# Optimization experiments

Measured on AMD Instinct MI355X. Metric: run time of the kernel, lower is better.

The kernel has to match this reference:

```python
import jax, jax.numpy as jnp
import numpy as np

MAX_NUM_CAPS = 10
NEG = -1e9

def _layernorm(x, g, b):
    m = x.mean(-1, keepdims=True)
    v = x.var(-1, keepdims=True)
    return (x - m) / jnp.sqrt(v + 1e-5) * g + b

def _gatv2(x, Wl, Wr, att, bias, adj):
    # x: [B,M,F]; Wl/Wr: [F,H*C]; att: [H,C]; adj: [B,M,M] bool, adj[b,i,j] = edge i->j
    B, M, F = x.shape
    H, C = att.shape
    xl = jnp.einsum('bmf,fhc->bmhc', x, Wl.reshape(F, H, C))  # source transform
    xr = jnp.einsum('bmf,fhc->bmhc', x, Wr.reshape(F, H, C))  # target transform
    # GATv2 score: att . leaky_relu(xl[i] + xr[j]) for edge (src=i, dst=j)
    z = jax.nn.leaky_relu(xl[:, :, None, :, :] + xr[:, None, :, :, :], 0.2)  # [B,i,j,H,C]
    e = jnp.einsum('bijhc,hc->bijh', z, att)
    e = jnp.where(adj[..., None], e, NEG)
    alpha = jax.nn.softmax(e, axis=1)  # softmax over incoming sources i per target j
    out = jnp.einsum('bijh,bihc->bjhc', alpha, xl)  # aggregate at targets
    return out.reshape(B, M, H * C) + bias

def setup_inputs() -> dict:
    key = jax.random.key(0)
    ks = jax.random.split(key, 16)
    B, N, T = 128, 16, 48
    Fm, H, C3 = 128, 4, 64
    s = 0.05
    inp = {
        'team_obs': jax.random.normal(ks[0], (B, N, 14), jnp.float32),
        'target_obs': jax.random.normal(ks[1], (B, T, 15), jnp.float32),
        'team_mask': jax.random.normal(ks[2], (B, 2, N), jnp.float32),
        'local_target_mask': jnp.ones((B, T + 1), jnp.float32),
        'W_emb': jax.random.normal(ks[3], (16, Fm), jnp.float32) * s,
        'b_emb': jnp.zeros((Fm,), jnp.float32),
        'Wl1': jax.random.normal(ks[4], (Fm, Fm), jnp.float32) * s,
        'Wr1': jax.random.normal(ks[5], (Fm, Fm), jnp.float32) * s,
        'att1': jax.random.normal(ks[6], (H, Fm // H), jnp.float32) * s,
        'b1': jnp.zeros((Fm,), jnp.float32),
        'Wl2': jax.random.normal(ks[7], (Fm, Fm), jnp.float32) * s,
        'Wr2': jax.random.normal(ks[8], (Fm, Fm), jnp.float32) * s,
        'att2': jax.random.normal(ks[9], (H, Fm // H), jnp.float32) * s,
        'b2': jnp.zeros((Fm,), jnp.float32),
        'Wl3': jax.random.normal(ks[10], (Fm, C3), jnp.float32) * s,
        'Wr3': jax.random.normal(ks[11], (Fm, C3), jnp.float32) * s,
        'att3': jax.random.normal(ks[12], (1, C3), jnp.float32) * s,
        'b3': jnp.zeros((C3,), jnp.float32),
        'ln1_g': jnp.ones((Fm,), jnp.float32),
        'ln1_b': jnp.zeros((Fm,), jnp.float32),
        'ln2_g': jnp.ones((Fm,), jnp.float32),
        'ln2_b': jnp.zeros((Fm,), jnp.float32),
    }
    return inp

def reference(team_obs, target_obs, team_mask, local_target_mask,
              W_emb, b_emb, Wl1, Wr1, att1, b1, Wl2, Wr2, att2, b2,
              Wl3, Wr3, att3, b3, ln1_g, ln1_b, ln2_g, ln2_b):
    B, N, _ = team_obs.shape
    team = jnp.concatenate([team_obs, jnp.zeros((B, N, 2), team_obs.dtype)], axis=2)
    tgt = target_obs[:, :, :-1]
    T = tgt.shape[1]
    tgt = jnp.concatenate([tgt[:, :, :2 + MAX_NUM_CAPS],
                           jnp.zeros((B, T, 2), tgt.dtype),
                           tgt[:, :, -2:]], axis=2)
    fin = jnp.concatenate([team, tgt], axis=1)  # [B, M, inp_dim]
    h = fin @ W_emb + b_emb  # [B, M, 128]
    imp_team = team_mask[:, 0] != -1e9          # [B, N]
    imp_tgt = local_target_mask[:, :-1] != 0.0  # [B, T]
    imp = jnp.concatenate([imp_team, imp_tgt], axis=1)  # [B, M]
    M = N + T
    eye = jnp.eye(M, dtype=bool)
    # edges among active nodes minus diagonal; PyG GATv2Conv add_self_loops=True re-adds self edges
    adj = (imp[:, :, None] & imp[:, None, :] & ~eye) | eye  # [B, M, M]
    out = jax.nn.relu(_layernorm(_gatv2(h, Wl1, Wr1, att1, b1, adj), ln1_g, ln1_b))
    out = jax.nn.relu(_layernorm(_gatv2(out, Wl2, Wr2, att2, b2, adj), ln2_g, ln2_b))
    out = _gatv2(out, Wl3, Wr3, att3, b3, adj)
    return out  # [B, M, out_dim]
```

## Files before the change

kernel.cpp:

```cpp
#include <hip/hip_runtime.h>

typedef unsigned short u16;
typedef unsigned int   u32;
typedef _Float16 h2  __attribute__((ext_vector_type(2)));
typedef __fp16   hw2 __attribute__((ext_vector_type(2)));
typedef __fp16   hw8 __attribute__((ext_vector_type(8)));
typedef float    f4  __attribute__((ext_vector_type(4)));

#define XS 136
#define PS 72
#define BS 72
#define OS 72

static __device__ __forceinline__ h2 pk(float a, float b) {
    return __builtin_bit_cast(h2, __builtin_amdgcn_cvt_pkrtz(a, b));
}
static __device__ __forceinline__ float dot2(h2 a, h2 b, float c) {
    return __builtin_amdgcn_fdot2(__builtin_bit_cast(hw2, a),
                                  __builtin_bit_cast(hw2, b), c, false);
}
static __device__ __forceinline__ h2  b2h(u32 v) { return __builtin_bit_cast(h2, v); }
static __device__ __forceinline__ u32 h2u(h2 v)  { return __builtin_bit_cast(u32, v); }
static __device__ __forceinline__ h2  abs2(h2 v) { return b2h(h2u(v) & 0x7fff7fffu); }
static __device__ __forceinline__ u16 f2h(float f) { return __builtin_bit_cast(u16, (_Float16)f); }
static __device__ __forceinline__ f4 mfma16(uint4 a, uint4 b, f4 c) {
    return __builtin_amdgcn_mfma_f32_16x16x32_f16(__builtin_bit_cast(hw8, a),
                                                  __builtin_bit_cast(hw8, b), c, 0, 0, 0);
}

__global__ void pack_weights(const float* __restrict__ Wl1, const float* __restrict__ Wr1,
                             const float* __restrict__ Wl2, const float* __restrict__ Wr2,
                             const float* __restrict__ Wl3, const float* __restrict__ Wr3,
                             u32* __restrict__ wpk)
{
    const int o = blockIdx.x * 256 + threadIdx.x;
    const float* src; u32* dst; int local; int N;
    if      (o < 8192)  { src = Wl1; dst = wpk;         local = o;         N = 128; }
    else if (o < 16384) { src = Wr1; dst = wpk + 8192;  local = o - 8192;  N = 128; }
    else if (o < 24576) { src = Wl2; dst = wpk + 16384; local = o - 16384; N = 128; }
    else if (o < 32768) { src = Wr2; dst = wpk + 24576; local = o - 24576; N = 128; }
    else if (o < 36864) { src = Wl3; dst = wpk + 32768; local = o - 32768; N = 64;  }
    else                { src = Wr3; dst = wpk + 36864; local = o - 36864; N = 64;  }
    const int i2   = local & 3;
    const int lane = (local >> 2) & 63;
    const int frag = local >> 8;
    const int kb   = frag & 3;
    const int nt   = frag >> 2;
    const int k0   = kb*32 + ((lane >> 4) << 3) + i2*2;
    const int n    = nt*16 + (lane & 15);
    dst[local] = h2u(pk(src[k0*N + n], src[(k0+1)*N + n]));
}

static __device__ __forceinline__ void compute_imp(int t, int b,
    const float* __restrict__ team_mask, const float* __restrict__ ltm, float* sImp)
{
    if (t < 64) {
        float im;
        if (t < 16) im = (team_mask[b*32 + t] != -1000000000.0f) ? 1.f : 0.f;
        else        im = (ltm[b*49 + (t-16)] != 0.0f) ? 1.f : 0.f;
        sImp[t] = im;
    }
}

static __device__ __forceinline__ void matmul128(int w, int lane,
    const u32* __restrict__ wpkL, const u32* __restrict__ wpkR,
    const u16* sX, u16* sXl, uint4* sXrP, u16* sXlB)
{
    const int  mt  = w & 3;
    const bool isR = (w >= 4);
    const u32* wp  = isR ? wpkR : wpkL;
    const int  n15 = lane & 15;
    const int  qd  = lane >> 4;
    uint4 afr[4];
#pragma unroll
    for (int kb = 0; kb < 4; kb++)
        afr[kb] = *(const uint4*)&sX[(mt*16 + n15)*XS + kb*32 + (qd << 3)];
#pragma unroll
    for (int nt = 0; nt < 8; nt++) {
        f4 acc = {0.f, 0.f, 0.f, 0.f};
#pragma unroll
        for (int kb = 0; kb < 4; kb++) {
            uint4 bf = *(const uint4*)&wp[((nt*4 + kb)*64 + lane)*4];
            acc = mfma16(afr[kb], bf, acc);
        }
        const int n  = nt*16 + n15;
        const int mb = mt*16 + (qd << 2);
        if (!isR) {
#pragma unroll
            for (int r = 0; r < 4; r++) sXl[(mb + r)*XS + n] = f2h(acc[r]);
            uint2 u;
            u.x = h2u(pk(acc[0], acc[1]));
            u.y = h2u(pk(acc[2], acc[3]));
            *(uint2*)&sXlB[n*BS + mb] = u;
        } else {
            u16* xp = (u16*)sXrP;
#pragma unroll
            for (int r = 0; r < 4; r++)
                xp[(((n >> 3)*64) + mb + r)*8 + (n & 7)] = f2h(acc[r]);
        }
    }
}

static __device__ __forceinline__ void attn_scores(int w, int lane,
    const float* __restrict__ att,
    const u16* sXl, const uint4* sXrP, u16* sP,
    float* sAl, float* sL2, const float* sImp)
{
    const int h  = w & 3;
    const int hf = w >> 2;
    const int j  = lane;

    h2 a2[16];
#pragma unroll
    for (int q = 0; q < 16; q++) a2[q] = pk(att[h*32 + 2*q], att[h*32 + 2*q + 1]);

    if (w < 4) {
        const uint4* pr = (const uint4*)&sXl[lane*XS + h*32];
        float al = 0.f;
#pragma unroll
        for (int c4 = 0; c4 < 4; c4++) {
            uint4 v = pr[c4];
            al = dot2(b2h(v.x), a2[c4*4+0], al);
            al = dot2(b2h(v.y), a2[c4*4+1], al);
            al = dot2(b2h(v.z), a2[c4*4+2], al);
            al = dot2(b2h(v.w), a2[c4*4+3], al);
        }
        sAl[h*64 + lane] = al;
    }

    h2 xr2[16];
#pragma unroll
    for (int s = 0; s < 4; s++) {
        uint4 v = sXrP[(h*4 + s)*64 + j];
        xr2[s*4+0] = b2h(v.x); xr2[s*4+1] = b2h(v.y);
        xr2[s*4+2] = b2h(v.z); xr2[s*4+3] = b2h(v.w);
    }
    float Ar = 0.f;
#pragma unroll
    for (int q = 0; q < 16; q++) Ar = dot2(a2[q], xr2[q], Ar);
    const float impj = sImp[j];
    __syncthreads();

    float l = 0.f;
    uint4* pd = (uint4*)&sP[(h*64 + j)*PS + hf*32];
    for (int c8 = 0; c8 < 4; c8++) {
        u32 pr4[4];
        float pprev = 0.f;
#pragma unroll
        for (int i2 = 0; i2 < 8; i2++) {
            const int i = hf*32 + c8*8 + i2;
            const uint4* pl = (const uint4*)&sXl[i*XS + h*32];
            uint4 v0 = pl[0], v1 = pl[1], v2 = pl[2], v3 = pl[3];
            h2 xl2[16];
            xl2[0] = b2h(v0.x); xl2[1] = b2h(v0.y); xl2[2]  = b2h(v0.z); xl2[3]  = b2h(v0.w);
            xl2[4] = b2h(v1.x); xl2[5] = b2h(v1.y); xl2[6]  = b2h(v1.z); xl2[7]  = b2h(v1.w);
            xl2[8] = b2h(v2.x); xl2[9] = b2h(v2.y); xl2[10] = b2h(v2.z); xl2[11] = b2h(v2.w);
            xl2[12]= b2h(v3.x); xl2[13]= b2h(v3.y); xl2[14] = b2h(v3.z); xl2[15] = b2h(v3.w);
            float S0 = 0.f, S1 = 0.f;
#pragma unroll
            for (int q = 0; q < 16; q += 2) {
                h2 t0 = abs2(xl2[q]   + xr2[q]);
                h2 t1 = abs2(xl2[q+1] + xr2[q+1]);
                S0 = dot2(a2[q],   t0, S0);
                S1 = dot2(a2[q+1], t1, S1);
            }
            float e  = 0.6f*(sAl[h*64 + i] + Ar) + 0.4f*(S0 + S1);
            float ad = (i == j) ? 1.f : impj * sImp[i];
            float p  = (ad != 0.f) ? __expf(e) : 0.f;
            if (i2 & 1) {
                h2 pp = pk(pprev, p);
                pr4[i2 >> 1] = h2u(pp);
                l += (float)pp[0] + (float)pp[1];
            } else {
                pprev = p;
            }
        }
        pd[c8] = make_uint4(pr4[0], pr4[1], pr4[2], pr4[3]);
    }
    sL2[h*128 + hf*64 + j] = l;
}

static __device__ __forceinline__ void attn_agg_ln(int w, int lane,
    const float* __restrict__ bias, const float* __restrict__ lg, const float* __restrict__ lb,
    const u16* sP, const u16* sXlB, float* sOutF, const float* sL2,
    float* sPart, u16* sXout)
{
    const int h   = w & 3;
    const int jh2 = w >> 2;
    const int n15 = lane & 15;
    const int kq  = lane >> 4;

    f4 acc00 = {0.f,0.f,0.f,0.f}, acc01 = acc00, acc10 = acc00, acc11 = acc00;
#pragma unroll
    for (int ks = 0; ks < 2; ks++) {
        uint4 af0 = *(const uint4*)&sP[(h*64 + (jh2*2+0)*16 + n15)*PS + ks*32 + kq*8];
        uint4 af1 = *(const uint4*)&sP[(h*64 + (jh2*2+1)*16 + n15)*PS + ks*32 + kq*8];
        uint4 bf0 = *(const uint4*)&sXlB[(h*32 +  0 + n15)*BS + ks*32 + kq*8];
        uint4 bf1 = *(const uint4*)&sXlB[(h*32 + 16 + n15)*BS + ks*32 + kq*8];
        acc00 = mfma16(af0, bf0, acc00);
        acc01 = mfma16(af0, bf1, acc01);
        acc10 = mfma16(af1, bf0, acc10);
        acc11 = mfma16(af1, bf1, acc11);
    }
    {
        const int jb0 = jh2*32 + kq*4;
#pragma unroll
        for (int r = 0; r < 4; r++) {
            sOutF[(h*32 +  0 + n15)*OS + jb0 + r]      = acc00[r];
            sOutF[(h*32 + 16 + n15)*OS + jb0 + r]      = acc01[r];
            sOutF[(h*32 +  0 + n15)*OS + jb0 + 16 + r] = acc10[r];
            sOutF[(h*32 + 16 + n15)*OS + jb0 + 16 + r] = acc11[r];
        }
    }
    __syncthreads();

    const int cg = w, j = lane, hh = w >> 1;
    const float l  = sL2[hh*128 + j] + sL2[hh*128 + 64 + j];
    const float rl = 1.f / l;
    float y[16];
    float s1 = 0.f, s2 = 0.f;
#pragma unroll
    for (int k = 0; k < 16; k++) {
        float v = fmaf(sOutF[(cg*16 + k)*OS + j], rl, bias[cg*16 + k]);
        y[k] = v; s1 += v; s2 = fmaf(v, v, s2);
    }
    sPart[cg*64 + j] = s1;
    sPart[512 + cg*64 + j] = s2;
    __syncthreads();
    float su = 0.f, sq = 0.f;
#pragma unroll
    for (int p = 0; p < 8; p++) { su += sPart[p*64 + j]; sq += sPart[512 + p*64 + j]; }
    const float mean = su * 0.0078125f;
    const float var  = sq * 0.0078125f - mean*mean;
    const float rstd = rsqrtf(var + 1e-5f);
    u32* xo = (u32*)&sXout[j*XS];
#pragma unroll
    for (int q = 0; q < 8; q++) {
        const int c0 = cg*16 + 2*q;
        float v0 = fmaxf(fmaf((y[2*q]   - mean)*rstd, lg[c0],   lb[c0]),   0.f);
        float v1 = fmaxf(fmaf((y[2*q+1] - mean)*rstd, lg[c0+1], lb[c0+1]), 0.f);
        xo[cg*8 + q] = h2u(pk(v0, v1));
    }
}

__global__ void __launch_bounds__(512, 1) gnn_fused(
    const float* __restrict__ team_obs, const float* __restrict__ target_obs,
    const float* __restrict__ team_mask, const float* __restrict__ ltm,
    const float* __restrict__ W_emb, const float* __restrict__ b_emb,
    const float* __restrict__ att1, const float* __restrict__ b1,
    const float* __restrict__ ln1_g, const float* __restrict__ ln1_b,
    const float* __restrict__ att2, const float* __restrict__ b2,
    const float* __restrict__ ln2_g, const float* __restrict__ ln2_b,
    const float* __restrict__ att3, const float* __restrict__ b3,
    const u32* __restrict__ wpk, float* __restrict__ out)
{
    __shared__ __align__(16) u16   sX  [64*XS];
    __shared__ __align__(16) u16   sXl [64*XS];
    __shared__ __align__(16) uint4 sXrP[1024];
    __shared__ __align__(16) u16   sXlB[128*BS];
    __shared__ __align__(16) u16   sP  [4*64*PS];
    __shared__ __align__(16) float sOutF[128*OS];
    __shared__ float sAl [256];
    __shared__ float sPart[1024];
    __shared__ float sL2 [768];
    __shared__ float sImp[64];

    const int t    = threadIdx.x;
    const int w    = t >> 6;
    const int lane = t & 63;
    const int b    = blockIdx.x;

    float* sFin = (float*)sP;

    compute_imp(t, b, team_mask, ltm, sImp);
    for (int ee = t; ee < 1024; ee += 512) {
        int m = ee >> 4, k = ee & 15;
        float v = 0.f;
        if (m < 16) {
            if (k < 14) v = team_obs[(b*16 + m)*14 + k];
        } else {
            const float* tg = target_obs + (size_t)(b*48 + (m-16))*15;
            if      (k < 12)  v = tg[k];
            else if (k == 14) v = tg[12];
            else if (k == 15) v = tg[13];
        }
        sFin[m*16 + k] = v;
    }
    __syncthreads();

    {
        const int f = t & 127;
        const int g = t >> 7;
        float wreg[16];
#pragma unroll
        for (int k = 0; k < 16; k++) wreg[k] = W_emb[k*128 + f];
        const float bf = b_emb[f];
#pragma unroll
        for (int mm = 0; mm < 16; mm++) {
            int m = g*16 + mm;
            const float4* pf = (const float4*)&sFin[m*16];
            float4 f0 = pf[0], f1 = pf[1], f2 = pf[2], f3 = pf[3];
            float acc = bf;
            acc = fmaf(f0.x, wreg[0],  acc); acc = fmaf(f0.y, wreg[1],  acc);
            acc = fmaf(f0.z, wreg[2],  acc); acc = fmaf(f0.w, wreg[3],  acc);
            acc = fmaf(f1.x, wreg[4],  acc); acc = fmaf(f1.y, wreg[5],  acc);
            acc = fmaf(f1.z, wreg[6],  acc); acc = fmaf(f1.w, wreg[7],  acc);
            acc = fmaf(f2.x, wreg[8],  acc); acc = fmaf(f2.y, wreg[9],  acc);
            acc = fmaf(f2.z, wreg[10], acc); acc = fmaf(f2.w, wreg[11], acc);
            acc = fmaf(f3.x, wreg[12], acc); acc = fmaf(f3.y, wreg[13], acc);
            acc = fmaf(f3.z, wreg[14], acc); acc = fmaf(f3.w, wreg[15], acc);
            sX[m*XS + f] = f2h(acc);
        }
    }
    __syncthreads();

    matmul128(w, lane, wpk, wpk + 8192, sX, sXl, sXrP, sXlB);
    __syncthreads();
    attn_scores(w, lane, att1, sXl, sXrP, sP, sAl, sL2, sImp);
    __syncthreads();
    attn_agg_ln(w, lane, b1, ln1_g, ln1_b, sP, sXlB, sOutF, sL2, sPart, sX);
    __syncthreads();

    matmul128(w, lane, wpk + 16384, wpk + 24576, sX, sXl, sXrP, sXlB);
    __syncthreads();
    attn_scores(w, lane, att2, sXl, sXrP, sP, sAl, sL2, sImp);
    __syncthreads();
    attn_agg_ln(w, lane, b2, ln2_g, ln2_b, sP, sXlB, sOutF, sL2, sPart, sX);
    __syncthreads();

    {
        const int  mt  = w & 3;
        const bool isR = (w >= 4);
        const u32* wp  = isR ? (wpk + 36864) : (wpk + 32768);
        const int  n15 = lane & 15;
        const int  qd  = lane >> 4;
        uint4 afr[4];
#pragma unroll
        for (int kb = 0; kb < 4; kb++)
            afr[kb] = *(const uint4*)&sX[(mt*16 + n15)*XS + kb*32 + (qd << 3)];
#pragma unroll
        for (int nt = 0; nt < 4; nt++) {
            f4 acc = {0.f, 0.f, 0.f, 0.f};
#pragma unroll
            for (int kb = 0; kb < 4; kb++) {
                uint4 bf = *(const uint4*)&wp[((nt*4 + kb)*64 + lane)*4];
                acc = mfma16(afr[kb], bf, acc);
            }
            const int n  = nt*16 + n15;
            const int mb = mt*16 + (qd << 2);
            if (!isR) {
#pragma unroll
                for (int r = 0; r < 4; r++) sXl[(mb + r)*XS + n] = f2h(acc[r]);
                uint2 u;
                u.x = h2u(pk(acc[0], acc[1]));
                u.y = h2u(pk(acc[2], acc[3]));
                *(uint2*)&sXlB[n*BS + mb] = u;
            } else {
                u16* xp = (u16*)sXrP;
#pragma unroll
                for (int r = 0; r < 4; r++)
                    xp[(((n >> 3)*64) + mb + r)*8 + (n & 7)] = f2h(acc[r]);
            }
        }
    }
    __syncthreads();

    {
        h2 a2l[4];
#pragma unroll
        for (int q = 0; q < 4; q++) a2l[q] = pk(att3[w*8 + 2*q], att3[w*8 + 2*q + 1]);
        uint4 v = *(const uint4*)&sXl[lane*XS + w*8];
        float al = 0.f;
        al = dot2(b2h(v.x), a2l[0], al);
        al = dot2(b2h(v.y), a2l[1], al);
        al = dot2(b2h(v.z), a2l[2], al);
        al = dot2(b2h(v.w), a2l[3], al);
        sPart[w*64 + lane] = al;
    }
    __syncthreads();
    if (t < 64) {
        sAl[t] = ((sPart[t] + sPart[64+t]) + (sPart[128+t] + sPart[192+t]))
               + ((sPart[256+t] + sPart[320+t]) + (sPart[384+t] + sPart[448+t]));
    }
    __syncthreads();

    {
        h2 a3[32], xr3[32];
#pragma unroll
        for (int q = 0; q < 32; q++) a3[q] = pk(att3[2*q], att3[2*q + 1]);
#pragma unroll
        for (int s = 0; s < 8; s++) {
            uint4 v = sXrP[s*64 + lane];
            xr3[s*4+0] = b2h(v.x); xr3[s*4+1] = b2h(v.y);
            xr3[s*4+2] = b2h(v.z); xr3[s*4+3] = b2h(v.w);
        }
        float Ar = 0.f;
#pragma unroll
        for (int q = 0; q < 32; q++) Ar = dot2(a3[q], xr3[q], Ar);
        const float impj = sImp[lane];
        float l3 = 0.f;
        u32 pr4[4];
        float pprev = 0.f;
#pragma unroll
        for (int ii = 0; ii < 8; ii++) {
            const int i = w*8 + ii;
            const uint4* pl = (const uint4*)&sXl[i*XS];
            float S0 = 0.f, S1 = 0.f;
#pragma unroll
            for (int c4 = 0; c4 < 8; c4++) {
                uint4 v = pl[c4];
                S0 = dot2(a3[c4*4+0], abs2(b2h(v.x) + xr3[c4*4+0]), S0);
                S1 = dot2(a3[c4*4+1], abs2(b2h(v.y) + xr3[c4*4+1]), S1);
                S0 = dot2(a3[c4*4+2], abs2(b2h(v.z) + xr3[c4*4+2]), S0);
                S1 = dot2(a3[c4*4+3], abs2(b2h(v.w) + xr3[c4*4+3]), S1);
            }
            float e  = 0.6f*(sAl[i] + Ar) + 0.4f*(S0 + S1);
            float ad = (i == lane) ? 1.f : impj * sImp[i];
            float p  = (ad != 0.f) ? __expf(e) : 0.f;
            if (ii & 1) {
                h2 pp = pk(pprev, p);
                pr4[ii >> 1] = h2u(pp);
                l3 += (float)pp[0] + (float)pp[1];
            } else {
                pprev = p;
            }
        }
        *(uint4*)&sP[lane*PS + w*8] = make_uint4(pr4[0], pr4[1], pr4[2], pr4[3]);
        sPart[w*64 + lane] = l3;
    }
    __syncthreads();
    if (t < 64) {
        float s = ((sPart[t] + sPart[64+t]) + (sPart[128+t] + sPart[192+t]))
                + ((sPart[256+t] + sPart[320+t]) + (sPart[384+t] + sPart[448+t]));
        sL2[t] = 1.f / s;
    }

    {
        const int jt  = w & 3;
        const int cth = w >> 2;
        const int n15 = lane & 15;
        const int kq  = lane >> 4;
        f4 acc0 = {0.f,0.f,0.f,0.f}, acc1 = acc0;
#pragma unroll
        for (int ks = 0; ks < 2; ks++) {
            uint4 af = *(const uint4*)&sP[(jt*16 + n15)*PS + ks*32 + kq*8];
            uint4 bf0 = *(const uint4*)&sXlB[((cth*2+0)*16 + n15)*BS + ks*32 + kq*8];
            uint4 bf1 = *(const uint4*)&sXlB[((cth*2+1)*16 + n15)*BS + ks*32 + kq*8];
            acc0 = mfma16(af, bf0, acc0);
            acc1 = mfma16(af, bf1, acc1);
        }
        __syncthreads();
        const int c0 = (cth*2+0)*16 + n15;
        const int c1 = (cth*2+1)*16 + n15;
        const float bc0 = b3[c0], bc1 = b3[c1];
#pragma unroll
        for (int r = 0; r < 4; r++) {
            const int jj = jt*16 + kq*4 + r;
            const float rl = sL2[jj];
            out[(size_t)b*4096 + (size_t)jj*64 + c0] = fmaf(acc0[r], rl, bc0);
            out[(size_t)b*4096 + (size_t)jj*64 + c1] = fmaf(acc1[r], rl, bc1);
        }
    }
}

extern "C" void kernel_launch(void* const* d_in, const int* in_sizes, int n_in,
                              void* d_out, int out_size, void* d_ws, size_t ws_size,
                              hipStream_t stream) {
    (void)in_sizes; (void)n_in; (void)ws_size; (void)out_size;
    const float* team_obs          = (const float*)d_in[0];
    const float* target_obs        = (const float*)d_in[1];
    const float* team_mask         = (const float*)d_in[2];
    const float* local_target_mask = (const float*)d_in[3];
    const float* W_emb             = (const float*)d_in[4];
    const float* b_emb             = (const float*)d_in[5];
    const float* Wl1               = (const float*)d_in[6];
    const float* Wr1               = (const float*)d_in[7];
    const float* att1              = (const float*)d_in[8];
    const float* b1                = (const float*)d_in[9];
    const float* Wl2               = (const float*)d_in[10];
    const float* Wr2               = (const float*)d_in[11];
    const float* att2              = (const float*)d_in[12];
    const float* b2                = (const float*)d_in[13];
    const float* Wl3               = (const float*)d_in[14];
    const float* Wr3               = (const float*)d_in[15];
    const float* att3              = (const float*)d_in[16];
    const float* b3                = (const float*)d_in[17];
    const float* ln1_g             = (const float*)d_in[18];
    const float* ln1_b             = (const float*)d_in[19];
    const float* ln2_g             = (const float*)d_in[20];
    const float* ln2_b             = (const float*)d_in[21];
    float* out = (float*)d_out;

    u32* wpk = (u32*)d_ws;

    pack_weights<<<dim3(160), dim3(256), 0, stream>>>(Wl1, Wr1, Wl2, Wr2, Wl3, Wr3, wpk);
    gnn_fused<<<dim3(128), dim3(512), 0, stream>>>(
        team_obs, target_obs, team_mask, local_target_mask, W_emb, b_emb,
        att1, b1, ln1_g, ln1_b, att2, b2, ln2_g, ln2_b, att3, b3, wpk, out);
}
```

Measured before the change: 143.3 us.

## Split fused GNN into per-layer kernels with target-row quarter blocks

Replaces the single fused 128-block kernel with three per-layer kernels, each launched over 512 blocks, where each block handles 16 target nodes of a graph. Intermediate activations are stored as fp16 in global memory, using the output buffer and workspace as scratch between layers. The aim is to fill more of the GPU's compute units than one block per graph allows. In exchange, each block recomputes the full source projection (Xl) for its graph, which is 4x redundant matmul work, and there are extra kernel launches and global round trips.

```diff
diff --git a/kernel.cpp b/kernel.cpp
--- a/kernel.cpp
+++ b/kernel.cpp
@@ -10,7 +10,7 @@
 #define XS 136
 #define PS 72
 #define BS 72
-#define OS 72
+#define OS2 20
 
 static __device__ __forceinline__ h2 pk(float a, float b) {
     return __builtin_bit_cast(h2, __builtin_amdgcn_cvt_pkrtz(a, b));
@@ -62,21 +62,27 @@
     }
 }
 
-static __device__ __forceinline__ void matmul128(int w, int lane,
-    const u32* __restrict__ wpkL, const u32* __restrict__ wpkR,
-    const u16* sX, u16* sXl, uint4* sXrP, u16* sXlB)
-{
-    const int  mt  = w & 3;
-    const bool isR = (w >= 4);
-    const u32* wp  = isR ? wpkR : wpkL;
-    const int  n15 = lane & 15;
-    const int  qd  = lane >> 4;
-    uint4 afr[4];
+static __device__ __forceinline__ void load_afr_lds(const u16* sX, int mt, int lane, uint4 afr[4]) {
+    const int n15 = lane & 15, qd = lane >> 4;
 #pragma unroll
     for (int kb = 0; kb < 4; kb++)
         afr[kb] = *(const uint4*)&sX[(mt*16 + n15)*XS + kb*32 + (qd << 3)];
-#pragma unroll
-    for (int nt = 0; nt < 8; nt++) {
+}
+static __device__ __forceinline__ void load_afr_glb(const u32* __restrict__ gxRow, int mt, int lane, uint4 afr[4]) {
+    const int n15 = lane & 15, qd = lane >> 4;
+    const int m = mt*16 + n15;
+#pragma unroll
+    for (int kb = 0; kb < 4; kb++)
+        afr[kb] = *(const uint4*)&gxRow[m*64 + kb*16 + qd*4];
+}
+
+static __device__ __forceinline__ void projL128(int w, int lane, const u32* __restrict__ wp,
+    const uint4 afr[4], u16* sXl, u16* sXlB)
+{
+    const int mt = w & 3, nh = w >> 2;
+    const int n15 = lane & 15, qd = lane >> 4;
+#pragma unroll
+    for (int nt = nh*4; nt < nh*4 + 4; nt++) {
         f4 acc = {0.f, 0.f, 0.f, 0.f};
 #pragma unroll
         for (int kb = 0; kb < 4; kb++) {
@@ -85,30 +91,42 @@
         }
         const int n  = nt*16 + n15;
         const int mb = mt*16 + (qd << 2);
-        if (!isR) {
-#pragma unroll
-            for (int r = 0; r < 4; r++) sXl[(mb + r)*XS + n] = f2h(acc[r]);
-            uint2 u;
-            u.x = h2u(pk(acc[0], acc[1]));
-            u.y = h2u(pk(acc[2], acc[3]));
-            *(uint2*)&sXlB[n*BS + mb] = u;
-        } else {
-            u16* xp = (u16*)sXrP;
-#pragma unroll
-            for (int r = 0; r < 4; r++)
-                xp[(((n >> 3)*64) + mb + r)*8 + (n & 7)] = f2h(acc[r]);
-        }
-    }
-}
-
-static __device__ __forceinline__ void attn_scores(int w, int lane,
+#pragma unroll
+        for (int r = 0; r < 4; r++) sXl[(mb + r)*XS + n] = f2h(acc[r]);
+        uint2 u;
+        u.x = h2u(pk(acc[0], acc[1]));
+        u.y = h2u(pk(acc[2], acc[3]));
+        *(uint2*)&sXlB[n*BS + mb] = u;
+    }
+}
+
+static __device__ __forceinline__ void projR16(int w, int lane, const u32* __restrict__ wp,
+    const uint4 afq[4], u16* sXrPx)
+{
+    const int n15 = lane & 15, qd = lane >> 4;
+    const int nt = w;
+    f4 acc = {0.f, 0.f, 0.f, 0.f};
+#pragma unroll
+    for (int kb = 0; kb < 4; kb++) {
+        uint4 bf = *(const uint4*)&wp[((nt*4 + kb)*64 + lane)*4];
+        acc = mfma16(afq[kb], bf, acc);
+    }
+    const int n = nt*16 + n15;
+#pragma unroll
+    for (int r = 0; r < 4; r++)
+        sXrPx[((n >> 3)*16 + (qd << 2) + r)*8 + (n & 7)] = f2h(acc[r]);
+}
+
+static __device__ __forceinline__ void scores16(int w, int lane, int j0,
     const float* __restrict__ att,
-    const u16* sXl, const uint4* sXrP, u16* sP,
+    const u16* sXl, const u16* sXrPx, u16* sP,
     float* sAl, float* sL2, const float* sImp)
 {
     const int h  = w & 3;
-    const int hf = w >> 2;
-    const int j  = lane;
+    const int qh = w >> 2;
+    const int jj = lane & 15;
+    const int is = lane >> 4;
+    const int j  = j0 + jj;
 
     h2 a2[16];
 #pragma unroll
@@ -131,7 +149,7 @@
     h2 xr2[16];
 #pragma unroll
     for (int s = 0; s < 4; s++) {
-        uint4 v = sXrP[(h*4 + s)*64 + j];
+        uint4 v = *(const uint4*)&sXrPx[((h*4 + s)*16 + jj)*8];
         xr2[s*4+0] = b2h(v.x); xr2[s*4+1] = b2h(v.y);
         xr2[s*4+2] = b2h(v.z); xr2[s*4+3] = b2h(v.w);
     }
@@ -142,135 +160,122 @@
     __syncthreads();
 
     float l = 0.f;
-    uint4* pd = (uint4*)&sP[(h*64 + j)*PS + hf*32];
-    for (int c8 = 0; c8 < 4; c8++) {
-        u32 pr4[4];
-        float pprev = 0.f;
-#pragma unroll
-        for (int i2 = 0; i2 < 8; i2++) {
-            const int i = hf*32 + c8*8 + i2;
-            const uint4* pl = (const uint4*)&sXl[i*XS + h*32];
-            uint4 v0 = pl[0], v1 = pl[1], v2 = pl[2], v3 = pl[3];
-            h2 xl2[16];
-            xl2[0] = b2h(v0.x); xl2[1] = b2h(v0.y); xl2[2]  = b2h(v0.z); xl2[3]  = b2h(v0.w);
-            xl2[4] = b2h(v1.x); xl2[5] = b2h(v1.y); xl2[6]  = b2h(v1.z); xl2[7]  = b2h(v1.w);
-            xl2[8] = b2h(v2.x); xl2[9] = b2h(v2.y); xl2[10] = b2h(v2.z); xl2[11] = b2h(v2.w);
-            xl2[12]= b2h(v3.x); xl2[13]= b2h(v3.y); xl2[14] = b2h(v3.z); xl2[15] = b2h(v3.w);
-            float S0 = 0.f, S1 = 0.f;
-#pragma unroll
-            for (int q = 0; q < 16; q += 2) {
-                h2 t0 = abs2(xl2[q]   + xr2[q]);
-                h2 t1 = abs2(xl2[q+1] + xr2[q+1]);
-                S0 = dot2(a2[q],   t0, S0);
-                S1 = dot2(a2[q+1], t1, S1);
-            }
-            float e  = 0.6f*(sAl[h*64 + i] + Ar) + 0.4f*(S0 + S1);
-            float ad = (i == j) ? 1.f : impj * sImp[i];
-            float p  = (ad != 0.f) ? __expf(e) : 0.f;
-            if (i2 & 1) {
-                h2 pp = pk(pprev, p);
-                pr4[i2 >> 1] = h2u(pp);
-                l += (float)pp[0] + (float)pp[1];
-            } else {
-                pprev = p;
-            }
-        }
-        pd[c8] = make_uint4(pr4[0], pr4[1], pr4[2], pr4[3]);
-    }
-    sL2[h*128 + hf*64 + j] = l;
-}
-
-static __device__ __forceinline__ void attn_agg_ln(int w, int lane,
+    u32 pr4[4];
+    float pprev = 0.f;
+#pragma unroll
+    for (int i2 = 0; i2 < 8; i2++) {
+        const int i = qh*32 + is*8 + i2;
+        const uint4* pl = (const uint4*)&sXl[i*XS + h*32];
+        uint4 v0 = pl[0], v1 = pl[1], v2 = pl[2], v3 = pl[3];
+        h2 xl2[16];
+        xl2[0] = b2h(v0.x); xl2[1] = b2h(v0.y); xl2[2]  = b2h(v0.z); xl2[3]  = b2h(v0.w);
+        xl2[4] = b2h(v1.x); xl2[5] = b2h(v1.y); xl2[6]  = b2h(v1.z); xl2[7]  = b2h(v1.w);
+        xl2[8] = b2h(v2.x); xl2[9] = b2h(v2.y); xl2[10] = b2h(v2.z); xl2[11] = b2h(v2.w);
+        xl2[12]= b2h(v3.x); xl2[13]= b2h(v3.y); xl2[14] = b2h(v3.z); xl2[15] = b2h(v3.w);
+        float S0 = 0.f, S1 = 0.f;
+#pragma unroll
+        for (int q = 0; q < 16; q += 2) {
+            h2 t0 = abs2(xl2[q]   + xr2[q]);
+            h2 t1 = abs2(xl2[q+1] + xr2[q+1]);
+            S0 = dot2(a2[q],   t0, S0);
+            S1 = dot2(a2[q+1], t1, S1);
+        }
+        float e  = 0.6f*(sAl[h*64 + i] + Ar) + 0.4f*(S0 + S1);
+        float ad = (i == j) ? 1.f : impj * sImp[i];
+        float p  = (ad != 0.f) ? __expf(e) : 0.f;
+        if (i2 & 1) {
+            h2 pp = pk(pprev, p);
+            pr4[i2 >> 1] = h2u(pp);
+            l += (float)pp[0] + (float)pp[1];
+        } else {
+            pprev = p;
+        }
+    }
+    *(uint4*)&sP[(h*16 + jj)*PS + qh*32 + is*8] = make_uint4(pr4[0], pr4[1], pr4[2], pr4[3]);
+    sL2[((h*2 + qh)*4 + is)*16 + jj] = l;
+}
+
+static __device__ __forceinline__ void aggln16(int w, int lane, int b, int j0,
     const float* __restrict__ bias, const float* __restrict__ lg, const float* __restrict__ lb,
     const u16* sP, const u16* sXlB, float* sOutF, const float* sL2,
-    float* sPart, u16* sXout)
+    float* sPart, u32* __restrict__ gxOut)
 {
     const int h   = w & 3;
-    const int jh2 = w >> 2;
+    const int cb  = w >> 2;
     const int n15 = lane & 15;
     const int kq  = lane >> 4;
 
-    f4 acc00 = {0.f,0.f,0.f,0.f}, acc01 = acc00, acc10 = acc00, acc11 = acc00;
+    f4 acc = {0.f,0.f,0.f,0.f};
 #pragma unroll
     for (int ks = 0; ks < 2; ks++) {
-        uint4 af0 = *(const uint4*)&sP[(h*64 + (jh2*2+0)*16 + n15)*PS + ks*32 + kq*8];
-        uint4 af1 = *(const uint4*)&sP[(h*64 + (jh2*2+1)*16 + n15)*PS + ks*32 + kq*8];
-        uint4 bf0 = *(const uint4*)&sXlB[(h*32 +  0 + n15)*BS + ks*32 + kq*8];
-        uint4 bf1 = *(const uint4*)&sXlB[(h*32 + 16 + n15)*BS + ks*32 + kq*8];
-        acc00 = mfma16(af0, bf0, acc00);
-        acc01 = mfma16(af0, bf1, acc01);
-        acc10 = mfma16(af1, bf0, acc10);
-        acc11 = mfma16(af1, bf1, acc11);
-    }
-    {
-        const int jb0 = jh2*32 + kq*4;
-#pragma unroll
-        for (int r = 0; r < 4; r++) {
-            sOutF[(h*32 +  0 + n15)*OS + jb0 + r]      = acc00[r];
-            sOutF[(h*32 + 16 + n15)*OS + jb0 + r]      = acc01[r];
-            sOutF[(h*32 +  0 + n15)*OS + jb0 + 16 + r] = acc10[r];
-            sOutF[(h*32 + 16 + n15)*OS + jb0 + 16 + r] = acc11[r];
-        }
-    }
-    __syncthreads();
-
-    const int cg = w, j = lane, hh = w >> 1;
-    const float l  = sL2[hh*128 + j] + sL2[hh*128 + 64 + j];
+        uint4 af = *(const uint4*)&sP[(h*16 + n15)*PS + ks*32 + kq*8];
+        uint4 bf = *(const uint4*)&sXlB[(h*32 + cb*16 + n15)*BS + ks*32 + kq*8];
+        acc = mfma16(af, bf, acc);
+    }
+#pragma unroll
+    for (int r = 0; r < 4; r++)
+        sOutF[(h*32 + cb*16 + n15)*OS2 + kq*4 + r] = acc[r];
+    __syncthreads();
+
+    const int jj = lane & 15, is2 = lane >> 4, hd = w >> 1;
+    float l = 0.f;
+#pragma unroll
+    for (int g = 0; g < 8; g++) l += sL2[(hd*8 + g)*16 + jj];
     const float rl = 1.f / l;
-    float y[16];
+    const int c0 = w*16 + is2*4;
+    float y[4];
     float s1 = 0.f, s2 = 0.f;
 #pragma unroll
-    for (int k = 0; k < 16; k++) {
-        float v = fmaf(sOutF[(cg*16 + k)*OS + j], rl, bias[cg*16 + k]);
+    for (int k = 0; k < 4; k++) {
+        float v = fmaf(sOutF[(c0 + k)*OS2 + jj], rl, bias[c0 + k]);
         y[k] = v; s1 += v; s2 = fmaf(v, v, s2);
     }
-    sPart[cg*64 + j] = s1;
-    sPart[512 + cg*64 + j] = s2;
+    sPart[(w*4 + is2)*16 + jj]       = s1;
+    sPart[512 + (w*4 + is2)*16 + jj] = s2;
     __syncthreads();
     float su = 0.f, sq = 0.f;
 #pragma unroll
-    for (int p = 0; p < 8; p++) { su += sPart[p*64 + j]; sq += sPart[512 + p*64 + j]; }
+    for (int g = 0; g < 32; g++) { su += sPart[g*16 + jj]; sq += sPart[512 + g*16 + jj]; }
     const float mean = su * 0.0078125f;
     const float var  = sq * 0.0078125f - mean*mean;
     const float rstd = rsqrtf(var + 1e-5f);
-    u32* xo = (u32*)&sXout[j*XS];
-#pragma unroll
-    for (int q = 0; q < 8; q++) {
-        const int c0 = cg*16 + 2*q;
-        float v0 = fmaxf(fmaf((y[2*q]   - mean)*rstd, lg[c0],   lb[c0]),   0.f);
-        float v1 = fmaxf(fmaf((y[2*q+1] - mean)*rstd, lg[c0+1], lb[c0+1]), 0.f);
-        xo[cg*8 + q] = h2u(pk(v0, v1));
-    }
-}
-
-__global__ void __launch_bounds__(512, 1) gnn_fused(
+    float v0 = fmaxf(fmaf((y[0] - mean)*rstd, lg[c0],   lb[c0]),   0.f);
+    float v1 = fmaxf(fmaf((y[1] - mean)*rstd, lg[c0+1], lb[c0+1]), 0.f);
+    float v2 = fmaxf(fmaf((y[2] - mean)*rstd, lg[c0+2], lb[c0+2]), 0.f);
+    float v3 = fmaxf(fmaf((y[3] - mean)*rstd, lg[c0+3], lb[c0+3]), 0.f);
+    uint2 o;
+    o.x = h2u(pk(v0, v1));
+    o.y = h2u(pk(v2, v3));
+    *(uint2*)(gxOut + (size_t)b*4096 + (size_t)(j0 + jj)*64 + (c0 >> 1)) = o;
+}
+
+__global__ void __launch_bounds__(512, 4) gnn_l1(
     const float* __restrict__ team_obs, const float* __restrict__ target_obs,
     const float* __restrict__ team_mask, const float* __restrict__ ltm,
     const float* __restrict__ W_emb, const float* __restrict__ b_emb,
     const float* __restrict__ att1, const float* __restrict__ b1,
     const float* __restrict__ ln1_g, const float* __restrict__ ln1_b,
-    const float* __restrict__ att2, const float* __restrict__ b2,
-    const float* __restrict__ ln2_g, const float* __restrict__ ln2_b,
-    const float* __restrict__ att3, const float* __restrict__ b3,
-    const u32* __restrict__ wpk, float* __restrict__ out)
-{
-    __shared__ __align__(16) u16   sX  [64*XS];
-    __shared__ __align__(16) u16   sXl [64*XS];
-    __shared__ __align__(16) uint4 sXrP[1024];
-    __shared__ __align__(16) u16   sXlB[128*BS];
-    __shared__ __align__(16) u16   sP  [4*64*PS];
-    __shared__ __align__(16) float sOutF[128*OS];
+    const u32* __restrict__ wpk, u32* __restrict__ gx1)
+{
+    __shared__ __align__(16) u16 sX   [64*XS];
+    __shared__ __align__(16) u16 sXl  [64*XS];
+    __shared__ __align__(16) u16 sXlB [128*BS];
+    __shared__ __align__(16) u16 sXrPx[2048];
+    __shared__ __align__(16) u16 sP   [4*16*PS];
     __shared__ float sAl [256];
+    __shared__ float sL2 [512];
     __shared__ float sPart[1024];
-    __shared__ float sL2 [768];
     __shared__ float sImp[64];
 
     const int t    = threadIdx.x;
     const int w    = t >> 6;
     const int lane = t & 63;
-    const int b    = blockIdx.x;
-
-    float* sFin = (float*)sP;
+    const int b    = blockIdx.x & 127;
+    const int q    = blockIdx.x >> 7;
+    const int j0   = q*16;
+
+    float* sFin  = (float*)sP;
+    float* sOutF = (float*)sX;
 
     compute_imp(t, b, team_mask, ltm, sImp);
     for (int ee = t; ee < 1024; ee += 512) {
@@ -314,33 +319,90 @@
     }
     __syncthreads();
 
-    matmul128(w, lane, wpk, wpk + 8192, sX, sXl, sXrP, sXlB);
-    __syncthreads();
-    attn_scores(w, lane, att1, sXl, sXrP, sP, sAl, sL2, sImp);
-    __syncthreads();
-    attn_agg_ln(w, lane, b1, ln1_g, ln1_b, sP, sXlB, sOutF, sL2, sPart, sX);
-    __syncthreads();
-
-    matmul128(w, lane, wpk + 16384, wpk + 24576, sX, sXl, sXrP, sXlB);
-    __syncthreads();
-    attn_scores(w, lane, att2, sXl, sXrP, sP, sAl, sL2, sImp);
-    __syncthreads();
-    attn_agg_ln(w, lane, b2, ln2_g, ln2_b, sP, sXlB, sOutF, sL2, sPart, sX);
-    __syncthreads();
+    uint4 afr[4], afq[4];
+    load_afr_lds(sX, w & 3, lane, afr);
+    load_afr_lds(sX, q,     lane, afq);
+    projL128(w, lane, wpk,        afr, sXl, sXlB);
+    projR16 (w, lane, wpk + 8192, afq, sXrPx);
+    __syncthreads();
+
+    scores16(w, lane, j0, att1, sXl, sXrPx, sP, sAl, sL2, sImp);
+    __syncthreads();
+    aggln16(w, lane, b, j0, b1, ln1_g, ln1_b, sP, sXlB, sOutF, sL2, sPart, gx1);
+}
+
+__global__ void __launch_bounds__(512, 4) gnn_l2(
+    const float* __restrict__ team_mask, const float* __restrict__ ltm,
+    const float* __restrict__ att2, const float* __restrict__ b2,
+    const float* __restrict__ ln2_g, const float* __restrict__ ln2_b,
+    const u32* __restrict__ wpk, const u32* __restrict__ gxIn, u32* __restrict__ gxOut)
+{
+    __shared__ __align__(16) u16 sXl  [64*XS];
+    __shared__ __align__(16) u16 sXlB [128*BS];
+    __shared__ __align__(16) u16 sXrPx[2048];
+    __shared__ __align__(16) u16 sP   [4*16*PS];
+    __shared__ __align__(16) float sOutF[128*OS2];
+    __shared__ float sAl [256];
+    __shared__ float sL2 [512];
+    __shared__ float sPart[1024];
+    __shared__ float sImp[64];
+
+    const int t    = threadIdx.x;
+    const int w    = t >> 6;
+    const int lane = t & 63;
+    const int b    = blockIdx.x & 127;
+    const int q    = blockIdx.x >> 7;
+    const int j0   = q*16;
+
+    compute_imp(t, b, team_mask, ltm, sImp);
+    const u32* gxRow = gxIn + (size_t)b*4096;
+
+    uint4 afr[4], afq[4];
+    load_afr_glb(gxRow, w & 3, lane, afr);
+    load_afr_glb(gxRow, q,     lane, afq);
+    projL128(w, lane, wpk + 16384, afr, sXl, sXlB);
+    projR16 (w, lane, wpk + 24576, afq, sXrPx);
+    __syncthreads();
+
+    scores16(w, lane, j0, att2, sXl, sXrPx, sP, sAl, sL2, sImp);
+    __syncthreads();
+    aggln16(w, lane, b, j0, b2, ln2_g, ln2_b, sP, sXlB, sOutF, sL2, sPart, gxOut);
+}
+
+__global__ void __launch_bounds__(512, 4) gnn_l3(
+    const float* __restrict__ team_mask, const float* __restrict__ ltm,
+    const float* __restrict__ att3, const float* __restrict__ b3,
+    const u32* __restrict__ wpk, const u32* __restrict__ gxIn, float* __restrict__ out)
+{
+    __shared__ __align__(16) u16 sXl3 [64*72];
+    __shared__ __align__(16) u16 sXlB3[64*72];
+    __shared__ __align__(16) u16 sXrP3[1024];
+    __shared__ __align__(16) u16 sP3  [16*72];
+    __shared__ float sAl3[64];
+    __shared__ float sPart[512];
+    __shared__ float sRl [16];
+    __shared__ float sImp[64];
+
+    const int t    = threadIdx.x;
+    const int w    = t >> 6;
+    const int lane = t & 63;
+    const int b    = blockIdx.x & 127;
+    const int q    = blockIdx.x >> 7;
+    const int j0   = q*16;
+    const int n15  = lane & 15;
+    const int qd   = lane >> 4;
+
+    compute_imp(t, b, team_mask, ltm, sImp);
+    const u32* gxRow = gxIn + (size_t)b*4096;
 
     {
-        const int  mt  = w & 3;
-        const bool isR = (w >= 4);
-        const u32* wp  = isR ? (wpk + 36864) : (wpk + 32768);
-        const int  n15 = lane & 15;
-        const int  qd  = lane >> 4;
         uint4 afr[4];
-#pragma unroll
-        for (int kb = 0; kb < 4; kb++)
-            afr[kb] = *(const uint4*)&sX[(mt*16 + n15)*XS + kb*32 + (qd << 3)];
-#pragma unroll
-        for (int nt = 0; nt < 4; nt++) {
-            f4 acc = {0.f, 0.f, 0.f, 0.f};
+        load_afr_glb(gxRow, w & 3, lane, afr);
+        const u32* wp = wpk + 32768;
+        const int mt = w & 3, nh = w >> 2;
+#pragma unroll
+        for (int nt = nh*2; nt < nh*2 + 2; nt++) {
+            f4 acc = {0.f,0.f,0.f,0.f};
 #pragma unroll
             for (int kb = 0; kb < 4; kb++) {
                 uint4 bf = *(const uint4*)&wp[((nt*4 + kb)*64 + lane)*4];
@@ -348,28 +410,36 @@
             }
             const int n  = nt*16 + n15;
             const int mb = mt*16 + (qd << 2);
-            if (!isR) {
-#pragma unroll
-                for (int r = 0; r < 4; r++) sXl[(mb + r)*XS + n] = f2h(acc[r]);
-                uint2 u;
-                u.x = h2u(pk(acc[0], acc[1]));
-                u.y = h2u(pk(acc[2], acc[3]));
-                *(uint2*)&sXlB[n*BS + mb] = u;
-            } else {
-                u16* xp = (u16*)sXrP;
-#pragma unroll
-                for (int r = 0; r < 4; r++)
-                    xp[(((n >> 3)*64) + mb + r)*8 + (n & 7)] = f2h(acc[r]);
-            }
-        }
+#pragma unroll
+            for (int r = 0; r < 4; r++) sXl3[(mb + r)*72 + n] = f2h(acc[r]);
+            uint2 u;
+            u.x = h2u(pk(acc[0], acc[1]));
+            u.y = h2u(pk(acc[2], acc[3]));
+            *(uint2*)&sXlB3[n*72 + mb] = u;
+        }
+    }
+    if (w < 4) {
+        uint4 afq[4];
+        load_afr_glb(gxRow, q, lane, afq);
+        const u32* wp = wpk + 36864;
+        f4 acc = {0.f,0.f,0.f,0.f};
+#pragma unroll
+        for (int kb = 0; kb < 4; kb++) {
+            uint4 bf = *(const uint4*)&wp[((w*4 + kb)*64 + lane)*4];
+            acc = mfma16(afq[kb], bf, acc);
+        }
+        const int n = w*16 + n15;
+#pragma unroll
+        for (int r = 0; r < 4; r++)
+            sXrP3[((n >> 3)*16 + (qd << 2) + r)*8 + (n & 7)] = f2h(acc[r]);
     }
     __syncthreads();
 
     {
         h2 a2l[4];
 #pragma unroll
-        for (int q = 0; q < 4; q++) a2l[q] = pk(att3[w*8 + 2*q], att3[w*8 + 2*q + 1]);
-        uint4 v = *(const uint4*)&sXl[lane*XS + w*8];
+        for (int qq = 0; qq < 4; qq++) a2l[qq] = pk(att3[w*8 + 2*qq], att3[w*8 + 2*qq + 1]);
+        uint4 v = *(const uint4*)&sXl3[lane*72 + w*8];
         float al = 0.f;
         al = dot2(b2h(v.x), a2l[0], al);
         al = dot2(b2h(v.y), a2l[1], al);
@@ -379,32 +449,34 @@
     }
     __syncthreads();
     if (t < 64) {
-        sAl[t] = ((sPart[t] + sPart[64+t]) + (sPart[128+t] + sPart[192+t]))
-               + ((sPart[256+t] + sPart[320+t]) + (sPart[384+t] + sPart[448+t]));
+        sAl3[t] = ((sPart[t] + sPart[64+t]) + (sPart[128+t] + sPart[192+t]))
+                + ((sPart[256+t] + sPart[320+t]) + (sPart[384+t] + sPart[448+t]));
     }
     __syncthreads();
 
     {
+        const int jj = n15;
+        const int is = qd;
+        const int j  = j0 + jj;
         h2 a3[32], xr3[32];
 #pragma unroll
-        for (int q = 0; q < 32; q++) a3[q] = pk(att3[2*q], att3[2*q + 1]);
+        for (int qq = 0; qq < 32; qq++) a3[qq] = pk(att3[2*qq], att3[2*qq + 1]);
 #pragma unroll
         for (int s = 0; s < 8; s++) {
-            uint4 v = sXrP[s*64 + lane];
+            uint4 v = *(const uint4*)&sXrP3[(s*16 + jj)*8];
             xr3[s*4+0] = b2h(v.x); xr3[s*4+1] = b2h(v.y);
             xr3[s*4+2] = b2h(v.z); xr3[s*4+3] = b2h(v.w);
         }
         float Ar = 0.f;
 #pragma unroll
-        for (int q = 0; q < 32; q++) Ar = dot2(a3[q], xr3[q], Ar);
-        const float impj = sImp[lane];
-        float l3 = 0.f;
-        u32 pr4[4];
-        float pprev = 0.f;
-#pragma unroll
-        for (int ii = 0; ii < 8; ii++) {
-            const int i = w*8 + ii;
-            const uint4* pl = (const uint4*)&sXl[i*XS];
+        for (int qq = 0; qq < 32; qq++) Ar = dot2(a3[qq], xr3[qq], Ar);
+        const float impj = sImp[j];
+        const int i0 = w*8 + is*2;
+
+        float p0, p1;
+        {
+            const int i = i0;
+            const uint4* pl = (const uint4*)&sXl3[i*72];
             float S0 = 0.f, S1 = 0.f;
 #pragma unroll
             for (int c4 = 0; c4 < 8; c4++) {
@@ -414,51 +486,55 @@
                 S0 = dot2(a3[c4*4+2], abs2(b2h(v.z) + xr3[c4*4+2]), S0);
                 S1 = dot2(a3[c4*4+3], abs2(b2h(v.w) + xr3[c4*4+3]), S1);
             }
-            float e  = 0.6f*(sAl[i] + Ar) + 0.4f*(S0 + S1);
-            float ad = (i == lane) ? 1.f : impj * sImp[i];
-            float p  = (ad != 0.f) ? __expf(e) : 0.f;
-            if (ii & 1) {
-                h2 pp = pk(pprev, p);
-                pr4[ii >> 1] = h2u(pp);
-                l3 += (float)pp[0] + (float)pp[1];
-            } else {
-                pprev = p;
+            float e  = 0.6f*(sAl3[i] + Ar) + 0.4f*(S0 + S1);
+            float ad = (i == j) ? 1.f : impj * sImp[i];
+            p0 = (ad != 0.f) ? __expf(e) : 0.f;
+        }
+        {
+            const int i = i0 + 1;
+            const uint4* pl = (const uint4*)&sXl3[i*72];
+            float S0 = 0.f, S1 = 0.f;
+#pragma unroll
+            for (int c4 = 0; c4 < 8; c4++) {
+                uint4 v = pl[c4];
+                S0 = dot2(a3[c4*4+0], abs2(b2h(v.x) + xr3[c4*4+0]), S0);
+                S1 = dot2(a3[c4*4+1], abs2(b2h(v.y) + xr3[c4*4+1]), S1);
+                S0 = dot2(a3[c4*4+2], abs2(b2h(v.z) + xr3[c4*4+2]), S0);
+                S1 = dot2(a3[c4*4+3], abs2(b2h(v.w) + xr3[c4*4+3]), S1);
             }
-        }
-        *(uint4*)&sP[lane*PS + w*8] = make_uint4(pr4[0], pr4[1], pr4[2], pr4[3]);
-        sPart[w*64 + lane] = l3;
-    }
-    __syncthreads();
-    if (t < 64) {
-        float s = ((sPart[t] + sPart[64+t]) + (sPart[128+t] + sPart[192+t]))
-                + ((sPart[256+t] + sPart[320+t]) + (sPart[384+t] + sPart[448+t]));
-        sL2[t] = 1.f / s;
-    }
-
-    {
-        const int jt  = w & 3;
-        const int cth = w >> 2;
-        const int n15 = lane & 15;
-        const int kq  = lane >> 4;
-        f4 acc0 = {0.f,0.f,0.f,0.f}, acc1 = acc0;
+            float e  = 0.6f*(sAl3[i] + Ar) + 0.4f*(S0 + S1);
+            float ad = (i == j) ? 1.f : impj * sImp[i];
+            p1 = (ad != 0.f) ? __expf(e) : 0.f;
+        }
+        h2 pp = pk(p0, p1);
+        *(u32*)&sP3[jj*72 + i0] = h2u(pp);
+        sPart[(w*4 + is)*16 + jj] = (float)pp[0] + (float)pp[1];
+    }
+    __syncthreads();
+    if (t < 16) {
+        float s = 0.f;
+#pragma unroll
+        for (int g = 0; g < 32; g++) s += sPart[g*16 + t];
+        sRl[t] = 1.f / s;
+    }
+
+    f4 acc3 = {0.f,0.f,0.f,0.f};
+    if (w < 4) {
 #pragma unroll
         for (int ks = 0; ks < 2; ks++) {
-            uint4 af = *(const uint4*)&sP[(jt*16 + n15)*PS + ks*32 + kq*8];
-            uint4 bf0 = *(const uint4*)&sXlB[((cth*2+0)*16 + n15)*BS + ks*32 + kq*8];
-            uint4 bf1 = *(const uint4*)&sXlB[((cth*2+1)*16 + n15)*BS + ks*32 + kq*8];
-            acc0 = mfma16(af, bf0, acc0);
-            acc1 = mfma16(af, bf1, acc1);
-        }
-        __syncthreads();
-        const int c0 = (cth*2+0)*16 + n15;
-        const int c1 = (cth*2+1)*16 + n15;
-        const float bc0 = b3[c0], bc1 = b3[c1];
+            uint4 af = *(const uint4*)&sP3[n15*72 + ks*32 + (lane >> 4)*8];
+            uint4 bf = *(const uint4*)&sXlB3[(w*16 + n15)*72 + ks*32 + (lane >> 4)*8];
+            acc3 = mfma16(af, bf, acc3);
+        }
+    }
+    __syncthreads();
+    if (w < 4) {
+        const int c  = w*16 + n15;
+        const float bc = b3[c];
 #pragma unroll
         for (int r = 0; r < 4; r++) {
-            const int jj = jt*16 + kq*4 + r;
-            const float rl = sL2[jj];
-            out[(size_t)b*4096 + (size_t)jj*64 + c0] = fmaf(acc0[r], rl, bc0);
-            out[(size_t)b*4096 + (size_t)jj*64 + c1] = fmaf(acc1[r], rl, bc1);
+            const int jl = (lane >> 4)*4 + r;
+            out[(size_t)b*4096 + (size_t)(j0 + jl)*64 + c] = fmaf(acc3[r], sRl[jl], bc);
         }
     }
 }
@@ -492,9 +568,15 @@
     float* out = (float*)d_out;
 
     u32* wpk = (u32*)d_ws;
+    u32* gx2 = (u32*)d_ws + 40960;
+    u32* gx1 = (u32*)d_out;
 
     pack_weights<<<dim3(160), dim3(256), 0, stream>>>(Wl1, Wr1, Wl2, Wr2, Wl3, Wr3, wpk);
-    gnn_fused<<<dim3(128), dim3(512), 0, stream>>>(
+    gnn_l1<<<dim3(512), dim3(512), 0, stream>>>(
         team_obs, target_obs, team_mask, local_target_mask, W_emb, b_emb,
-        att1, b1, ln1_g, ln1_b, att2, b2, ln2_g, ln2_b, att3, b3, wpk, out);
-}
+        att1, b1, ln1_g, ln1_b, wpk, gx1);
+    gnn_l2<<<dim3(512), dim3(512), 0, stream>>>(
+        team_mask, local_target_mask, att2, b2, ln2_g, ln2_b, wpk, gx1, gx2);
+    gnn_l3<<<dim3(512), dim3(512), 0, stream>>>(
+        team_mask, local_target_mask, att3, b3, wpk, gx2, out);
+}
```

Result: faster. 132.3 us, median of 2 (-7.7%).
